# Kernel tuning notes

Measured on AMD Instinct MI355X. Metric: run time of the kernel, lower is better.

## Reference

```python
import jax, jax.numpy as jnp
import numpy as np

B, S, D = 2, 2048, 2048
H, KVH, HD = 16, 8, 128
EPS = 1e-6
ROPE_THETA = 10000.0


def _rope_cache(seq_len, head_dim):
    inv_freq = 1.0 / (ROPE_THETA ** (np.arange(0, head_dim, 2, dtype=np.float32) / head_dim))
    t = np.arange(seq_len, dtype=np.float32)
    freqs = np.outer(t, inv_freq)                      # [S, HD/2]
    emb = np.concatenate([freqs, freqs], axis=-1)      # [S, HD]
    return jnp.asarray(np.cos(emb)), jnp.asarray(np.sin(emb))


def setup_inputs() -> dict:
    key = jax.random.key(0)
    ks = jax.random.split(key, 10)
    x = jax.random.normal(ks[0], (B, S, D), dtype=jnp.float32)
    wq_q = jax.random.randint(ks[1], (H * HD, D), -127, 128, dtype=jnp.int32)
    wk_q = jax.random.randint(ks[2], (KVH * HD, D), -127, 128, dtype=jnp.int32)
    wv_q = jax.random.randint(ks[3], (KVH * HD, D), -127, 128, dtype=jnp.int32)
    wo_q = jax.random.randint(ks[4], (D, H * HD), -127, 128, dtype=jnp.int32)
    # per-output-channel scales (realistic small magnitudes)
    wq_s = jax.random.uniform(ks[5], (H * HD,), minval=1e-3, maxval=2e-2)
    wk_s = jax.random.uniform(ks[6], (KVH * HD,), minval=1e-3, maxval=2e-2)
    wv_s = jax.random.uniform(ks[7], (KVH * HD,), minval=1e-3, maxval=2e-2)
    wo_s = jax.random.uniform(ks[8], (D,), minval=1e-3, maxval=2e-2)
    q_norm_w = jnp.ones((HD,), dtype=jnp.float32)
    k_norm_w = jnp.ones((HD,), dtype=jnp.float32)
    cos_cache, sin_cache = _rope_cache(S, HD)
    return {"x": x, "wq_q": wq_q, "wq_s": wq_s, "wk_q": wk_q, "wk_s": wk_s,
            "wv_q": wv_q, "wv_s": wv_s, "wo_q": wo_q, "wo_s": wo_s,
            "q_norm_w": q_norm_w, "k_norm_w": k_norm_w,
            "cos_cache": cos_cache, "sin_cache": sin_cache}


def _dequant_linear(x, wq, ws):
    # W8A16-style: dequantize int8 weight with per-channel scale, then GEMM
    w = wq.astype(jnp.float32) * ws[:, None]   # [out, in]
    return x @ w.T


def _rms_norm(x, w, eps=EPS):
    var = jnp.mean(x * x, axis=-1, keepdims=True)
    return x * jax.lax.rsqrt(var + eps) * w


def _rotate_half(x):
    x1, x2 = jnp.split(x, 2, axis=-1)
    return jnp.concatenate([-x2, x1], axis=-1)


def _apply_rope(q, k, cos, sin):
    # q: [B,S,H,HD], k: [B,S,KVH,HD]; cos/sin: [S,HD] -> broadcast over batch, heads
    cos = cos[None, :, None, :]
    sin = sin[None, :, None, :]
    q = q * cos + _rotate_half(q) * sin
    k = k * cos + _rotate_half(k) * sin
    return q, k


def reference(x, wq_q, wq_s, wk_q, wk_s, wv_q, wv_s, wo_q, wo_s,
              q_norm_w, k_norm_w, cos_cache, sin_cache):
    batch, seq_len, dim = x.shape
    q = _dequant_linear(x, wq_q, wq_s).reshape(batch, seq_len, H, HD)
    k = _dequant_linear(x, wk_q, wk_s).reshape(batch, seq_len, KVH, HD)
    v = _dequant_linear(x, wv_q, wv_s).reshape(batch, seq_len, KVH, HD)
    q = _rms_norm(q, q_norm_w)
    k = _rms_norm(k, k_norm_w)
    # first forward: cache is empty -> kv = current k,v
    q, k = _apply_rope(q, k, cos_cache[:seq_len], sin_cache[:seq_len])
    q = q.transpose(0, 2, 1, 3)   # [B,H,S,HD]
    k = k.transpose(0, 2, 1, 3)   # [B,KVH,S,HD]
    v = v.transpose(0, 2, 1, 3)
    rep = H // KVH
    k = jnp.repeat(k, rep, axis=1)  # GQA repeat_interleave -> [B,H,S,HD]
    v = jnp.repeat(v, rep, axis=1)
    scale = 1.0 / jnp.sqrt(jnp.asarray(HD, dtype=x.dtype))
    scores = jnp.einsum('bhqd,bhkd->bhqk', q, k) * scale
    causal = jnp.tril(jnp.ones((seq_len, seq_len), dtype=bool))
    scores = jnp.where(causal[None, None], scores, jnp.finfo(scores.dtype).min)
    attn = jax.nn.softmax(scores, axis=-1)
    out = jnp.einsum('bhqk,bhkd->bhqd', attn, v)
    out = out.transpose(0, 2, 1, 3).reshape(batch, seq_len, H * HD)
    return _dequant_linear(out, wo_q, wo_s)
```

## Files before the change

### kernel.cpp

```cpp
#include <hip/hip_runtime.h>


typedef __attribute__((ext_vector_type(4))) float floatx4;
typedef __attribute__((ext_vector_type(8))) short short8v;
typedef __attribute__((ext_vector_type(4))) short short4v;
typedef __attribute__((ext_vector_type(8))) unsigned short ushort8v;
typedef __attribute__((ext_vector_type(4))) unsigned short ushort4v;

#define DEVINL __device__ __forceinline__

constexpr int cB = 2, cS = 2048, cD = 2048, cH = 16, cKVH = 8, cHD = 128;
constexpr int cM = cB * cS;
constexpr int cNqkv = (cH + 2 * cKVH) * cHD;
constexpr float cEPS = 1e-6f;
constexpr float cSCALE = 0.08838834764831845f;

DEVINL unsigned short f2bf(float f) {
  unsigned u = __float_as_uint(f);
  unsigned r = ((u >> 16) & 1u) + 0x7FFFu;
  return (unsigned short)((u + r) >> 16);
}
DEVINL float bf2f(unsigned short h) { return __uint_as_float(((unsigned)h) << 16); }

DEVINL floatx4 mfma_bf16(short8v a, short8v b, floatx4 c) {
  return __builtin_amdgcn_mfma_f32_16x16x32_bf16(a, b, c, 0, 0, 0);
}

DEVINL floatx4 mfma_pv(short4v a, short4v b, floatx4 c) {
#if __has_builtin(__builtin_amdgcn_mfma_f32_16x16x16bf16_1k)
  return __builtin_amdgcn_mfma_f32_16x16x16bf16_1k(a, b, c, 0, 0, 0);
#else
  short8v a8 = {a[0], a[1], a[2], a[3], (short)0, (short)0, (short)0, (short)0};
  short8v b8 = {b[0], b[1], b[2], b[3], (short)0, (short)0, (short)0, (short)0};
  return __builtin_amdgcn_mfma_f32_16x16x32_bf16(a8, b8, c, 0, 0, 0);
#endif
}

DEVINL void gl_lds16(const void* g, void* l) {
  __builtin_amdgcn_global_load_lds(
      (const __attribute__((address_space(1))) void*)g,
      (__attribute__((address_space(3))) void*)l, 16, 0, 0);
}

__global__ void detect_dtype(const unsigned* __restrict__ x, int* __restrict__ flag) {
  __shared__ int cnt;
  if (threadIdx.x == 0) cnt = 0;
  __syncthreads();
  int c = 0;
  for (int i = threadIdx.x; i < 4096; i += 256) {
    unsigned e = (x[i] >> 7) & 0xFFu;
    c += (e >= 100u && e <= 142u) ? 1 : 0;
  }
  atomicAdd(&cnt, c);
  __syncthreads();
  if (threadIdx.x == 0) *flag = (cnt > 2457) ? 1 : 0;
}

__global__ void conv_x(const void* __restrict__ src, unsigned short* __restrict__ dst,
                       int n, const int* __restrict__ flag) {
  int i = (blockIdx.x * 256 + threadIdx.x) * 8;
  if (i >= n) return;
  if (*flag) {
    *(ushort8v*)(dst + i) = *(const ushort8v*)((const unsigned short*)src + i);
  } else {
    const float* s = (const float*)src;
    ushort8v o;
#pragma unroll
    for (int j = 0; j < 8; j++) o[j] = f2bf(s[i + j]);
    *(ushort8v*)(dst + i) = o;
  }
}

__global__ void conv_f32(const void* __restrict__ src, float* __restrict__ dst,
                         int n, const int* __restrict__ flag) {
  int i = blockIdx.x * 256 + threadIdx.x;
  if (i >= n) return;
  dst[i] = (*flag) ? bf2f(((const unsigned short*)src)[i]) : ((const float*)src)[i];
}

__global__ void conv_w(const int* __restrict__ w, unsigned short* __restrict__ dst, int n) {
  int i = (blockIdx.x * 256 + threadIdx.x) * 4;
  if (i >= n) return;
  int4 v = *(const int4*)(w + i);
  ushort4v o;
  o[0] = f2bf((float)v.x); o[1] = f2bf((float)v.y);
  o[2] = f2bf((float)v.z); o[3] = f2bf((float)v.w);
  *(ushort4v*)(dst + i) = o;
}

__global__ void out_conv(const float* __restrict__ of, void* __restrict__ dout,
                         int n, const int* __restrict__ flag) {
  int i = blockIdx.x * 256 + threadIdx.x;
  if (i >= n) return;
  float v = of[i];
  if (*flag) ((unsigned short*)dout)[i] = f2bf(v);
  else       ((float*)dout)[i] = v;
}

__global__ __launch_bounds__(256) void gemm_bt(
    const unsigned short* __restrict__ A, const unsigned short* __restrict__ Bw,
    const float* __restrict__ colscale, float* __restrict__ C,
    int M, int N, int K) {
  __shared__ unsigned short As[128 * 64];
  __shared__ unsigned short Bs[128 * 64];
  const int tid = threadIdx.x;
  const int lane = tid & 63, wave = tid >> 6;
  const int q = lane >> 4, l16 = lane & 15;
  const int m0 = blockIdx.y * 128, n0 = blockIdx.x * 128;
  const int wm = (wave & 1) * 64, wn = (wave >> 1) * 64;

  floatx4 acc[4][4] = {};

  int goff[4];
#pragma unroll
  for (int i = 0; i < 4; i++) {
    int s = (wave * 4 + i) * 64 + lane;
    int r = s >> 3, u = (s & 7) ^ (r & 7);
    goff[i] = r * K + u * 8;
  }
  const unsigned short* Ag = A + (size_t)m0 * K;
  const unsigned short* Bg = Bw + (size_t)n0 * K;

  for (int k0 = 0; k0 < K; k0 += 64) {
    __syncthreads();
#pragma unroll
    for (int i = 0; i < 4; i++)
      gl_lds16(Ag + k0 + goff[i], (char*)As + (wave * 4 + i) * 1024);
#pragma unroll
    for (int i = 0; i < 4; i++)
      gl_lds16(Bg + k0 + goff[i], (char*)Bs + (wave * 4 + i) * 1024);
    __syncthreads();
#pragma unroll
    for (int kk = 0; kk < 2; kk++) {
      short8v af[4], bf[4];
#pragma unroll
      for (int mt = 0; mt < 4; mt++) {
        int row = wm + mt * 16 + l16;
        af[mt] = *(const short8v*)(As + row * 64 + (((kk * 4 + q) ^ (l16 & 7)) * 8));
      }
#pragma unroll
      for (int nt = 0; nt < 4; nt++) {
        int row = wn + nt * 16 + l16;
        bf[nt] = *(const short8v*)(Bs + row * 64 + (((kk * 4 + q) ^ (l16 & 7)) * 8));
      }
#pragma unroll
      for (int mt = 0; mt < 4; mt++)
#pragma unroll
        for (int nt = 0; nt < 4; nt++)
          acc[mt][nt] = mfma_bf16(af[mt], bf[nt], acc[mt][nt]);
    }
  }
#pragma unroll
  for (int mt = 0; mt < 4; mt++) {
    int r0 = m0 + wm + mt * 16 + q * 4;
#pragma unroll
    for (int nt = 0; nt < 4; nt++) {
      int cn = n0 + wn + nt * 16 + l16;
      float sc = colscale[cn];
#pragma unroll
      for (int rg = 0; rg < 4; rg++)
        C[(size_t)(r0 + rg) * N + cn] = acc[mt][nt][rg] * sc;
    }
  }
}

__global__ __launch_bounds__(64) void rmsrope(
    const float* __restrict__ QKV, const float* __restrict__ cosc,
    const float* __restrict__ sinc, const float* __restrict__ nw,
    unsigned short* __restrict__ Qb, unsigned short* __restrict__ Kb) {
  const int t = threadIdx.x;
  const int row = blockIdx.x;
  const int hidx = blockIdx.y;
  const int sidx = row & (cS - 1);
  const int bi = row >> 11;
  const bool isq = hidx < cH;
  const int col = isq ? hidx * cHD : cH * cHD + (hidx - cH) * cHD;
  const float* src = QKV + (size_t)row * cNqkv + col;
  float x1 = src[t], x2 = src[t + 64];
  float ss = x1 * x1 + x2 * x2;
  ss += __shfl_xor(ss, 1);  ss += __shfl_xor(ss, 2);  ss += __shfl_xor(ss, 4);
  ss += __shfl_xor(ss, 8);  ss += __shfl_xor(ss, 16); ss += __shfl_xor(ss, 32);
  float inv = rsqrtf(ss * (1.0f / cHD) + cEPS);
  const float* w = nw + (isq ? 0 : cHD);
  float n1 = x1 * inv * w[t], n2 = x2 * inv * w[t + 64];
  float c1 = cosc[sidx * cHD + t], c2 = cosc[sidx * cHD + t + 64];
  float s1 = sinc[sidx * cHD + t], s2 = sinc[sidx * cHD + t + 64];
  float o1 = n1 * c1 - n2 * s1;
  float o2 = n2 * c2 + n1 * s2;
  unsigned short* dst = isq
      ? (Qb + ((size_t)(bi * cH + hidx) * cS + sidx) * cHD)
      : (Kb + ((size_t)(bi * cKVH + (hidx - cH)) * cS + sidx) * cHD);
  dst[t] = f2bf(o1);
  dst[t + 64] = f2bf(o2);
}

__global__ __launch_bounds__(256) void vtrans(const float* __restrict__ QKV,
                                              unsigned short* __restrict__ Vt) {
  __shared__ unsigned short tile[64][72];
  const int t = threadIdx.x;
  const int s0 = blockIdx.x * 64, d0 = blockIdx.y * 64, bi = blockIdx.z;
  {
    const int rr = t >> 2, c0 = (t & 3) * 16;
    const float* src = QKV + (size_t)(bi * cS + s0 + rr) * cNqkv
                       + (cH * cHD + cKVH * cHD) + d0 + c0;
#pragma unroll
    for (int j = 0; j < 16; j += 4) {
      float4 v = *(const float4*)(src + j);
      tile[rr][c0 + j + 0] = f2bf(v.x);
      tile[rr][c0 + j + 1] = f2bf(v.y);
      tile[rr][c0 + j + 2] = f2bf(v.z);
      tile[rr][c0 + j + 3] = f2bf(v.w);
    }
  }
  __syncthreads();
  {
    const int dd = t >> 2, sc0 = (t & 3) * 16;
    const int dglob = d0 + dd;
    const int kh = dglob >> 7, dh = dglob & 127;
    unsigned short* dst = Vt + ((size_t)(bi * cKVH + kh) * cHD + dh) * cS + s0 + sc0;
    ushort8v o0, o1;
#pragma unroll
    for (int j = 0; j < 8; j++) { o0[j] = tile[sc0 + j][dd]; o1[j] = tile[sc0 + 8 + j][dd]; }
    *(ushort8v*)dst = o0;
    *(ushort8v*)(dst + 8) = o1;
  }
}

__global__ __launch_bounds__(256, 2) void attn(
    const unsigned short* __restrict__ Qb, const unsigned short* __restrict__ Kb,
    const unsigned short* __restrict__ Vt, unsigned short* __restrict__ AO) {
  __shared__ unsigned short SM[32768];
  const int tid = threadIdx.x;
  const int lane = tid & 63, wv = tid >> 6;
  const int q = lane >> 4, l16 = lane & 15;
  const int bi = blockIdx.z, h = blockIdx.y;
  const int kh = h >> 1;
  const int qt = (int)gridDim.x - 1 - (int)blockIdx.x;
  const int q0 = qt * 64;
  const int q0w = q0 + wv * 16;

  const unsigned short* Qbase = Qb + ((size_t)(bi * cH + h) * cS + q0w) * cHD;
  const unsigned short* Kbase = Kb + ((size_t)(bi * cKVH + kh) * cS) * cHD;
  const unsigned short* Vbase = Vt + ((size_t)(bi * cKVH + kh) * cHD) * cS;

  short8v qa[4];
#pragma unroll
  for (int c = 0; c < 4; c++)
    qa[c] = *(const short8v*)(Qbase + (size_t)l16 * cHD + c * 32 + q * 8);

  floatx4 oacc[8] = {};
  float lp = 0.f;

  int koff[4], voff[4];
#pragma unroll
  for (int i = 0; i < 4; i++) {
    int s = (wv * 4 + i) * 64 + lane;
    int r = s >> 4, u = (s & 15) ^ (r & 15);
    koff[i] = r * cHD + u * 8;
    int d = s >> 3, uv = (s & 7) ^ (d & 7);
    voff[i] = d * cS + uv * 8;
  }

  auto stage = [&](int win) {
    const int buf = (win & 1) * 16384;
    const int kv0 = win * 64;
    unsigned short* Kdst = SM + buf + (wv * 4) * 512;
    unsigned short* Vdst = SM + buf + 8192 + (wv * 4) * 512;
#pragma unroll
    for (int i = 0; i < 4; i++)
      gl_lds16(Kbase + (size_t)kv0 * cHD + koff[i], Kdst + i * 512);
#pragma unroll
    for (int i = 0; i < 4; i++)
      gl_lds16(Vbase + (size_t)kv0 + voff[i], Vdst + i * 512);
  };

  stage(0);
  for (int win = 0; win <= qt; win++) {
    __syncthreads();
    if (win < qt) stage(win + 1);
    const unsigned short* Ks = SM + (win & 1) * 16384;
    const unsigned short* Vs = Ks + 8192;

    floatx4 sres[4] = {};
#pragma unroll
    for (int c = 0; c < 4; c++) {
      short8v kf[4];
#pragma unroll
      for (int ntk = 0; ntk < 4; ntk++)
        kf[ntk] = *(const short8v*)(Ks + (ntk * 16 + l16) * 128 + (((c * 4 + q) ^ l16) * 8));
#pragma unroll
      for (int ntk = 0; ntk < 4; ntk++)
        sres[ntk] = mfma_bf16(kf[ntk], qa[c], sres[ntk]);
    }

    const bool lastwin = (win == qt);
    short4v pa[4];
#pragma unroll
    for (int ntk = 0; ntk < 4; ntk++) {
#pragma unroll
      for (int rg = 0; rg < 4; rg++) {
        float e = __expf(sres[ntk][rg] * cSCALE);
        if (lastwin && (ntk * 16 + q * 4 + rg > wv * 16 + l16)) e = 0.f;
        lp += e;
        pa[ntk][rg] = (short)f2bf(e);
      }
    }

#pragma unroll
    for (int ntk = 0; ntk < 4; ntk++) {
#pragma unroll
      for (int db = 0; db < 8; db++) {
        short4v vb = *(const short4v*)(Vs + (db * 16 + l16) * 64 +
                       (((ntk * 2 + (q >> 1)) ^ (l16 & 7)) * 8 + (q & 1) * 4));
        oacc[db] = mfma_pv(pa[ntk], vb, oacc[db]);
      }
    }
  }

  float lf = lp;
  lf += __shfl_xor(lf, 16);
  lf += __shfl_xor(lf, 32);
  float li[4];
#pragma unroll
  for (int rg = 0; rg < 4; rg++) li[rg] = 1.0f / __shfl(lf, q * 4 + rg);

#pragma unroll
  for (int rg = 0; rg < 4; rg++) {
    int row = q0w + q * 4 + rg;
    unsigned short* dst = AO + (size_t)(bi * cS + row) * (cH * cHD) + h * cHD;
#pragma unroll
    for (int db = 0; db < 8; db++)
      dst[db * 16 + l16] = f2bf(oacc[db][rg] * li[rg]);
  }
}

extern "C" void kernel_launch(void* const* d_in, const int* in_sizes, int n_in,
                              void* d_out, int out_size, void* d_ws, size_t ws_size,
                              hipStream_t stream) {
  (void)in_sizes; (void)n_in; (void)out_size; (void)ws_size;
  char* ws = (char*)d_ws;
  size_t off = 0;
  auto alloc = [&](size_t bytes) -> char* {
    char* p = ws + off;
    off += (bytes + 255) & ~((size_t)255);
    return p;
  };
  int* flag            = (int*)alloc(256);
  float* cosf_         = (float*)alloc((size_t)cS * cHD * 4);
  float* sinf_         = (float*)alloc((size_t)cS * cHD * 4);
  float* nw            = (float*)alloc(256 * 4);
  float* scat          = (float*)alloc(4096 * 4);
  float* so            = (float*)alloc(2048 * 4);
  unsigned short* xb   = (unsigned short*)alloc((size_t)cM * cD * 2);
  unsigned short* wcat = (unsigned short*)alloc((size_t)cNqkv * cD * 2);
  unsigned short* wob  = (unsigned short*)alloc((size_t)cD * cH * cHD * 2);
  unsigned short* Qb   = (unsigned short*)alloc((size_t)cB * cH * cS * cHD * 2);
  unsigned short* Kb   = (unsigned short*)alloc((size_t)cB * cKVH * cS * cHD * 2);
  unsigned short* Vt   = (unsigned short*)alloc((size_t)cB * cKVH * cHD * cS * 2);
  char* big            = alloc((size_t)cM * cNqkv * 4);
  float* qkvf          = (float*)big;
  unsigned short* AO   = (unsigned short*)big;
  float* of            = (float*)(big + (size_t)cM * cNqkv * 2);

  detect_dtype<<<1, 256, 0, stream>>>((const unsigned*)d_in[0], flag);

  conv_x<<<(cM * cD / 8 + 255) / 256, 256, 0, stream>>>(d_in[0], xb, cM * cD, flag);
  conv_f32<<<(cS * cHD + 255) / 256, 256, 0, stream>>>(d_in[11], cosf_, cS * cHD, flag);
  conv_f32<<<(cS * cHD + 255) / 256, 256, 0, stream>>>(d_in[12], sinf_, cS * cHD, flag);
  conv_f32<<<1, 256, 0, stream>>>(d_in[9], nw, cHD, flag);
  conv_f32<<<1, 256, 0, stream>>>(d_in[10], nw + cHD, cHD, flag);
  conv_f32<<<8, 256, 0, stream>>>(d_in[2], scat, 2048, flag);
  conv_f32<<<4, 256, 0, stream>>>(d_in[4], scat + 2048, 1024, flag);
  conv_f32<<<4, 256, 0, stream>>>(d_in[6], scat + 3072, 1024, flag);
  conv_f32<<<8, 256, 0, stream>>>(d_in[8], so, 2048, flag);
  conv_w<<<(2048 * 2048 / 4 + 255) / 256, 256, 0, stream>>>((const int*)d_in[1], wcat, 2048 * 2048);
  conv_w<<<(1024 * 2048 / 4 + 255) / 256, 256, 0, stream>>>((const int*)d_in[3], wcat + (size_t)2048 * 2048, 1024 * 2048);
  conv_w<<<(1024 * 2048 / 4 + 255) / 256, 256, 0, stream>>>((const int*)d_in[5], wcat + (size_t)3072 * 2048, 1024 * 2048);
  conv_w<<<(2048 * 2048 / 4 + 255) / 256, 256, 0, stream>>>((const int*)d_in[7], wob, 2048 * 2048);

  gemm_bt<<<dim3(cNqkv / 128, cM / 128), 256, 0, stream>>>(xb, wcat, scat, qkvf, cM, cNqkv, cD);
  rmsrope<<<dim3(cM, cH + cKVH), 64, 0, stream>>>(qkvf, cosf_, sinf_, nw, Qb, Kb);
  vtrans<<<dim3(cS / 64, cKVH * cHD / 64, cB), 256, 0, stream>>>(qkvf, Vt);
  attn<<<dim3(cS / 64, cH, cB), 256, 0, stream>>>(Qb, Kb, Vt, AO);
  gemm_bt<<<dim3(cD / 128, cM / 128), 256, 0, stream>>>(AO, wob, so, of, cM, cD, cH * cHD);
  out_conv<<<(cM * cD + 255) / 256, 256, 0, stream>>>(of, d_out, cM * cD, flag);
}
```

Baseline: 435.9 us.

## Fuse RMSNorm, RoPE and V transpose into QKV GEMM epilogue; fuse output conversion

The QKV GEMM epilogue now does the per-head RMSNorm, RoPE rotation and V transpose directly from the accumulators. Tile columns line up with head boundaries, and partner halves are exchanged through shared memory. This removes the fp32 QKV intermediate round-trip to HBM and drops the separate rmsrope and vtrans kernels. The output GEMM writes the final dtype directly instead of running a separate conversion pass, and cos/sin are packed into one float2 table. The cost is a heavier epilogue with extra syncs and LDS use, plus the rotate-half partner being read back after a bf16 round.

After: 476.3 us. 1.09x slower.

```diff
diff --git a/kernel.cpp b/kernel.cpp
--- a/kernel.cpp
+++ b/kernel.cpp
@@ -88,19 +88,186 @@
   *(ushort4v*)(dst + i) = o;
 }
 
-__global__ void out_conv(const float* __restrict__ of, void* __restrict__ dout,
-                         int n, const int* __restrict__ flag) {
+__global__ void rope_pack(const void* __restrict__ cosc, const void* __restrict__ sinc,
+                          float2* __restrict__ tab, const int* __restrict__ flag) {
   int i = blockIdx.x * 256 + threadIdx.x;
-  if (i >= n) return;
-  float v = of[i];
-  if (*flag) ((unsigned short*)dout)[i] = f2bf(v);
-  else       ((float*)dout)[i] = v;
-}
-
-__global__ __launch_bounds__(256) void gemm_bt(
+  if (i >= cS * 64) return;
+  int s = i >> 6, t = i & 63;
+  int f = *flag;
+  float c = f ? bf2f(((const unsigned short*)cosc)[s * cHD + t])
+              : ((const float*)cosc)[s * cHD + t];
+  float sn = f ? bf2f(((const unsigned short*)sinc)[s * cHD + t])
+               : ((const float*)sinc)[s * cHD + t];
+  tab[i] = make_float2(c, sn);
+}
+
+__global__ __launch_bounds__(256) void gemm_qkv(
     const unsigned short* __restrict__ A, const unsigned short* __restrict__ Bw,
-    const float* __restrict__ colscale, float* __restrict__ C,
-    int M, int N, int K) {
+    const float* __restrict__ colscale, const float2* __restrict__ ropetab,
+    const float* __restrict__ nw, unsigned short* __restrict__ Qb,
+    unsigned short* __restrict__ Kb, unsigned short* __restrict__ Vt) {
+  __shared__ float4 smem4[2192];
+  char* smem = (char*)smem4;
+  unsigned short* As = (unsigned short*)smem;
+  unsigned short* Bs = As + 8192;
+  const int tid = threadIdx.x;
+  const int lane = tid & 63, wave = tid >> 6;
+  const int q = lane >> 4, l16 = lane & 15;
+  const int m0 = blockIdx.y * 128, n0 = blockIdx.x * 128;
+  const int wm = (wave & 1) * 64, wn = (wave >> 1) * 64;
+
+  floatx4 acc[4][4] = {};
+
+  int goff[4];
+#pragma unroll
+  for (int i = 0; i < 4; i++) {
+    int s = (wave * 4 + i) * 64 + lane;
+    int r = s >> 3, u = (s & 7) ^ (r & 7);
+    goff[i] = r * cD + u * 8;
+  }
+  const unsigned short* Ag = A + (size_t)m0 * cD;
+  const unsigned short* Bg = Bw + (size_t)n0 * cD;
+
+  for (int k0 = 0; k0 < cD; k0 += 64) {
+    __syncthreads();
+#pragma unroll
+    for (int i = 0; i < 4; i++)
+      gl_lds16(Ag + k0 + goff[i], (char*)As + (wave * 4 + i) * 1024);
+#pragma unroll
+    for (int i = 0; i < 4; i++)
+      gl_lds16(Bg + k0 + goff[i], (char*)Bs + (wave * 4 + i) * 1024);
+    __syncthreads();
+#pragma unroll
+    for (int kk = 0; kk < 2; kk++) {
+      short8v af[4], bf[4];
+#pragma unroll
+      for (int mt = 0; mt < 4; mt++) {
+        int row = wm + mt * 16 + l16;
+        af[mt] = *(const short8v*)(As + row * 64 + (((kk * 4 + q) ^ (l16 & 7)) * 8));
+      }
+#pragma unroll
+      for (int nt = 0; nt < 4; nt++) {
+        int row = wn + nt * 16 + l16;
+        bf[nt] = *(const short8v*)(Bs + row * 64 + (((kk * 4 + q) ^ (l16 & 7)) * 8));
+      }
+#pragma unroll
+      for (int mt = 0; mt < 4; mt++)
+#pragma unroll
+        for (int nt = 0; nt < 4; nt++)
+          acc[mt][nt] = mfma_bf16(af[mt], bf[nt], acc[mt][nt]);
+    }
+  }
+
+  float sc[4];
+#pragma unroll
+  for (int nt = 0; nt < 4; nt++) sc[nt] = colscale[n0 + wn + nt * 16 + l16];
+#pragma unroll
+  for (int mt = 0; mt < 4; mt++)
+#pragma unroll
+    for (int nt = 0; nt < 4; nt++)
+#pragma unroll
+      for (int rg = 0; rg < 4; rg++) acc[mt][nt][rg] *= sc[nt];
+
+  const int tile_n = blockIdx.x;
+  const int bi = m0 >> 11, sbase = m0 & (cS - 1);
+  __syncthreads();
+
+  if (tile_n >= 24) {
+    unsigned short* T = (unsigned short*)smem;
+#pragma unroll
+    for (int mt = 0; mt < 4; mt++)
+#pragma unroll
+      for (int nt = 0; nt < 4; nt++) {
+        short4v pk;
+#pragma unroll
+        for (int rg = 0; rg < 4; rg++) pk[rg] = (short)f2bf(acc[mt][nt][rg]);
+        *(short4v*)(T + (wn + nt * 16 + l16) * 136 + (wm + mt * 16 + q * 4)) = pk;
+      }
+    __syncthreads();
+    const int d = tid >> 1, sh = (tid & 1) * 64;
+    unsigned short* dst = Vt + ((size_t)(bi * cKVH + (tile_n - 24)) * cHD + d) * cS
+                          + sbase + sh;
+#pragma unroll
+    for (int j = 0; j < 8; j++)
+      *(ushort8v*)(dst + j * 8) = *(const ushort8v*)(T + d * 136 + sh + j * 8);
+  } else {
+    unsigned short* W = (unsigned short*)smem;
+    float* ssq  = (float*)(smem + 32768);
+    float* invs = (float*)(smem + 33792);
+
+    float sl[4][4];
+#pragma unroll
+    for (int mt = 0; mt < 4; mt++)
+#pragma unroll
+      for (int rg = 0; rg < 4; rg++) {
+        float s = 0.f;
+#pragma unroll
+        for (int nt = 0; nt < 4; nt++) s += acc[mt][nt][rg] * acc[mt][nt][rg];
+        s += __shfl_xor(s, 1); s += __shfl_xor(s, 2);
+        s += __shfl_xor(s, 4); s += __shfl_xor(s, 8);
+        sl[mt][rg] = s;
+      }
+    unsigned short* Wo = W + wave * 4096;
+#pragma unroll
+    for (int mt = 0; mt < 4; mt++)
+#pragma unroll
+      for (int nt = 0; nt < 4; nt++) {
+        short4v pk;
+#pragma unroll
+        for (int rg = 0; rg < 4; rg++) pk[rg] = (short)f2bf(acc[mt][nt][rg]);
+        *(short4v*)(Wo + (mt * 4 + nt) * 256 + lane * 4) = pk;
+      }
+    if (l16 == 0) {
+#pragma unroll
+      for (int mt = 0; mt < 4; mt++)
+#pragma unroll
+        for (int rg = 0; rg < 4; rg++)
+          ssq[((wave >> 1) & 1) * 128 + wm + mt * 16 + q * 4 + rg] = sl[mt][rg];
+    }
+    __syncthreads();
+    if (tid < 128)
+      invs[tid] = rsqrtf((ssq[tid] + ssq[128 + tid]) * (1.0f / cHD) + cEPS);
+    __syncthreads();
+
+    const unsigned short* Wp = W + (wave ^ 2) * 4096;
+    const int wn1 = wave >> 1;
+    const float* nwb = nw + (tile_n < 16 ? 0 : cHD);
+    float wown[4], wpar[4];
+#pragma unroll
+    for (int nt = 0; nt < 4; nt++) {
+      wown[nt] = nwb[wn1 * 64 + nt * 16 + l16];
+      wpar[nt] = nwb[(wn1 ^ 1) * 64 + nt * 16 + l16];
+    }
+    unsigned short* dstb = (tile_n < 16)
+        ? Qb + ((size_t)(bi * cH + tile_n) * cS) * cHD
+        : Kb + ((size_t)(bi * cKVH + (tile_n - 16)) * cS) * cHD;
+#pragma unroll
+    for (int mt = 0; mt < 4; mt++) {
+      float iv[4];
+#pragma unroll
+      for (int rg = 0; rg < 4; rg++) iv[rg] = invs[wm + mt * 16 + q * 4 + rg];
+#pragma unroll
+      for (int nt = 0; nt < 4; nt++) {
+        short4v pk = *(const short4v*)(Wp + (mt * 4 + nt) * 256 + lane * 4);
+#pragma unroll
+        for (int rg = 0; rg < 4; rg++) {
+          int srow = sbase + wm + mt * 16 + q * 4 + rg;
+          float2 cs = ropetab[srow * 64 + nt * 16 + l16];
+          float nown = acc[mt][nt][rg] * iv[rg] * wown[nt];
+          float npar = bf2f((unsigned short)pk[rg]) * iv[rg] * wpar[nt];
+          float o = wn1 == 0 ? nown * cs.x - npar * cs.y
+                             : nown * cs.x + npar * cs.y;
+          dstb[(size_t)srow * cHD + wn1 * 64 + nt * 16 + l16] = f2bf(o);
+        }
+      }
+    }
+  }
+}
+
+__global__ __launch_bounds__(256) void gemm_out(
+    const unsigned short* __restrict__ A, const unsigned short* __restrict__ Bw,
+    const float* __restrict__ colscale, void* __restrict__ Cout,
+    const int* __restrict__ flag, int M, int N, int K) {
   __shared__ unsigned short As[128 * 64];
   __shared__ unsigned short Bs[128 * 64];
   const int tid = threadIdx.x;
@@ -150,6 +317,7 @@
           acc[mt][nt] = mfma_bf16(af[mt], bf[nt], acc[mt][nt]);
     }
   }
+  const int f = *flag;
 #pragma unroll
   for (int mt = 0; mt < 4; mt++) {
     int r0 = m0 + wm + mt * 16 + q * 4;
@@ -158,71 +326,12 @@
       int cn = n0 + wn + nt * 16 + l16;
       float sc = colscale[cn];
 #pragma unroll
-      for (int rg = 0; rg < 4; rg++)
-        C[(size_t)(r0 + rg) * N + cn] = acc[mt][nt][rg] * sc;
-    }
-  }
-}
-
-__global__ __launch_bounds__(64) void rmsrope(
-    const float* __restrict__ QKV, const float* __restrict__ cosc,
-    const float* __restrict__ sinc, const float* __restrict__ nw,
-    unsigned short* __restrict__ Qb, unsigned short* __restrict__ Kb) {
-  const int t = threadIdx.x;
-  const int row = blockIdx.x;
-  const int hidx = blockIdx.y;
-  const int sidx = row & (cS - 1);
-  const int bi = row >> 11;
-  const bool isq = hidx < cH;
-  const int col = isq ? hidx * cHD : cH * cHD + (hidx - cH) * cHD;
-  const float* src = QKV + (size_t)row * cNqkv + col;
-  float x1 = src[t], x2 = src[t + 64];
-  float ss = x1 * x1 + x2 * x2;
-  ss += __shfl_xor(ss, 1);  ss += __shfl_xor(ss, 2);  ss += __shfl_xor(ss, 4);
-  ss += __shfl_xor(ss, 8);  ss += __shfl_xor(ss, 16); ss += __shfl_xor(ss, 32);
-  float inv = rsqrtf(ss * (1.0f / cHD) + cEPS);
-  const float* w = nw + (isq ? 0 : cHD);
-  float n1 = x1 * inv * w[t], n2 = x2 * inv * w[t + 64];
-  float c1 = cosc[sidx * cHD + t], c2 = cosc[sidx * cHD + t + 64];
-  float s1 = sinc[sidx * cHD + t], s2 = sinc[sidx * cHD + t + 64];
-  float o1 = n1 * c1 - n2 * s1;
-  float o2 = n2 * c2 + n1 * s2;
-  unsigned short* dst = isq
-      ? (Qb + ((size_t)(bi * cH + hidx) * cS + sidx) * cHD)
-      : (Kb + ((size_t)(bi * cKVH + (hidx - cH)) * cS + sidx) * cHD);
-  dst[t] = f2bf(o1);
-  dst[t + 64] = f2bf(o2);
-}
-
-__global__ __launch_bounds__(256) void vtrans(const float* __restrict__ QKV,
-                                              unsigned short* __restrict__ Vt) {
-  __shared__ unsigned short tile[64][72];
-  const int t = threadIdx.x;
-  const int s0 = blockIdx.x * 64, d0 = blockIdx.y * 64, bi = blockIdx.z;
-  {
-    const int rr = t >> 2, c0 = (t & 3) * 16;
-    const float* src = QKV + (size_t)(bi * cS + s0 + rr) * cNqkv
-                       + (cH * cHD + cKVH * cHD) + d0 + c0;
-#pragma unroll
-    for (int j = 0; j < 16; j += 4) {
-      float4 v = *(const float4*)(src + j);
-      tile[rr][c0 + j + 0] = f2bf(v.x);
-      tile[rr][c0 + j + 1] = f2bf(v.y);
-      tile[rr][c0 + j + 2] = f2bf(v.z);
-      tile[rr][c0 + j + 3] = f2bf(v.w);
-    }
-  }
-  __syncthreads();
-  {
-    const int dd = t >> 2, sc0 = (t & 3) * 16;
-    const int dglob = d0 + dd;
-    const int kh = dglob >> 7, dh = dglob & 127;
-    unsigned short* dst = Vt + ((size_t)(bi * cKVH + kh) * cHD + dh) * cS + s0 + sc0;
-    ushort8v o0, o1;
-#pragma unroll
-    for (int j = 0; j < 8; j++) { o0[j] = tile[sc0 + j][dd]; o1[j] = tile[sc0 + 8 + j][dd]; }
-    *(ushort8v*)dst = o0;
-    *(ushort8v*)(dst + 8) = o1;
+      for (int rg = 0; rg < 4; rg++) {
+        float v = acc[mt][nt][rg] * sc;
+        if (f) ((unsigned short*)Cout)[(size_t)(r0 + rg) * N + cn] = f2bf(v);
+        else   ((float*)Cout)[(size_t)(r0 + rg) * N + cn] = v;
+      }
+    }
   }
 }
 
@@ -346,8 +455,7 @@
     return p;
   };
   int* flag            = (int*)alloc(256);
-  float* cosf_         = (float*)alloc((size_t)cS * cHD * 4);
-  float* sinf_         = (float*)alloc((size_t)cS * cHD * 4);
+  float2* ropetab      = (float2*)alloc((size_t)cS * 64 * 8);
   float* nw            = (float*)alloc(256 * 4);
   float* scat          = (float*)alloc(4096 * 4);
   float* so            = (float*)alloc(2048 * 4);
@@ -357,16 +465,12 @@
   unsigned short* Qb   = (unsigned short*)alloc((size_t)cB * cH * cS * cHD * 2);
   unsigned short* Kb   = (unsigned short*)alloc((size_t)cB * cKVH * cS * cHD * 2);
   unsigned short* Vt   = (unsigned short*)alloc((size_t)cB * cKVH * cHD * cS * 2);
-  char* big            = alloc((size_t)cM * cNqkv * 4);
-  float* qkvf          = (float*)big;
-  unsigned short* AO   = (unsigned short*)big;
-  float* of            = (float*)(big + (size_t)cM * cNqkv * 2);
+  unsigned short* AO   = (unsigned short*)alloc((size_t)cM * cD * 2);
 
   detect_dtype<<<1, 256, 0, stream>>>((const unsigned*)d_in[0], flag);
 
   conv_x<<<(cM * cD / 8 + 255) / 256, 256, 0, stream>>>(d_in[0], xb, cM * cD, flag);
-  conv_f32<<<(cS * cHD + 255) / 256, 256, 0, stream>>>(d_in[11], cosf_, cS * cHD, flag);
-  conv_f32<<<(cS * cHD + 255) / 256, 256, 0, stream>>>(d_in[12], sinf_, cS * cHD, flag);
+  rope_pack<<<(cS * 64 + 255) / 256, 256, 0, stream>>>(d_in[11], d_in[12], ropetab, flag);
   conv_f32<<<1, 256, 0, stream>>>(d_in[9], nw, cHD, flag);
   conv_f32<<<1, 256, 0, stream>>>(d_in[10], nw + cHD, cHD, flag);
   conv_f32<<<8, 256, 0, stream>>>(d_in[2], scat, 2048, flag);
@@ -378,10 +482,9 @@
   conv_w<<<(1024 * 2048 / 4 + 255) / 256, 256, 0, stream>>>((const int*)d_in[5], wcat + (size_t)3072 * 2048, 1024 * 2048);
   conv_w<<<(2048 * 2048 / 4 + 255) / 256, 256, 0, stream>>>((const int*)d_in[7], wob, 2048 * 2048);
 
-  gemm_bt<<<dim3(cNqkv / 128, cM / 128), 256, 0, stream>>>(xb, wcat, scat, qkvf, cM, cNqkv, cD);
-  rmsrope<<<dim3(cM, cH + cKVH), 64, 0, stream>>>(qkvf, cosf_, sinf_, nw, Qb, Kb);
-  vtrans<<<dim3(cS / 64, cKVH * cHD / 64, cB), 256, 0, stream>>>(qkvf, Vt);
+  gemm_qkv<<<dim3(cNqkv / 128, cM / 128), 256, 0, stream>>>(
+      xb, wcat, scat, ropetab, nw, Qb, Kb, Vt);
   attn<<<dim3(cS / 64, cH, cB), 256, 0, stream>>>(Qb, Kb, Vt, AO);
-  gemm_bt<<<dim3(cD / 128, cM / 128), 256, 0, stream>>>(AO, wob, so, of, cM, cD, cH * cHD);
-  out_conv<<<(cM * cD + 255) / 256, 256, 0, stream>>>(of, d_out, cM * cD, flag);
-}
+  gemm_out<<<dim3(cD / 128, cM / 128), 256, 0, stream>>>(
+      AO, wob, so, d_out, flag, cM, cD, cH * cHD);
+}
```
